# Kernel tuning notes

Hardware: AMD Instinct MI355X
Metric: run time of the kernel (lower is better)

The kernel has to match this reference:

```python
import jax, jax.numpy as jnp
import numpy as np

B, H, W, DIM = 1, 256, 256, 192
HEADS = 6
K, DIL = 7, 2            # NAttention kernel / dilation
WS, DF = 8, 2            # stripe window size, anchor down factor
AWS = WS // DF           # anchor window size (4)
N1, N2 = WS * WS, AWS * AWS
L = H * W
CPB_HID = 512


def _nbr(size, k, d):
    # 1D neighborhood-attention neighbor indices with dilation (edge-clamped)
    i = np.arange(size); g = i % d; p = i // d
    gsize = size // d  # d divides size
    start = np.clip(p - k // 2, 0, gsize - k)
    nbr_p = start[:, None] + np.arange(k)[None, :]
    nbr = g[:, None] + d * nbr_p                    # absolute key index
    rb = nbr_p - p[:, None] + (k - 1)               # rpb index in [0, 2k-2]
    return nbr.astype(np.int32), rb.astype(np.int32)

NBR_H, RB_H = _nbr(H, K, DIL)
NBR_W, RB_W = _nbr(W, K, DIL)


def _na_attention(q, k, v, rpb):
    # q,k,v: (B, heads, H, W, hd); rpb: (heads, 2K-1, 2K-1)
    bias = rpb[:, RB_H, :]                          # (heads,H,K,2K-1)
    bias = jnp.take(bias, RB_W, axis=3)             # (heads,H,K,W,K)
    bias = jnp.transpose(bias, (0, 1, 3, 2, 4))     # (heads,H,W,K,K)
    logits = []
    for ki in range(K):
        kh = jnp.take(k, NBR_H[:, ki], axis=2)
        for kj in range(K):
            khw = jnp.take(kh, NBR_W[:, kj], axis=3)
            logits.append(jnp.einsum('bnhwc,bnhwc->bnhw', q, khw))
    a = jnp.stack(logits, axis=-1).reshape(*q.shape[:4], K, K) + bias[None]
    a = jax.nn.softmax(a.reshape(*q.shape[:4], K * K), axis=-1).reshape(*q.shape[:4], K, K)
    out = jnp.zeros_like(q)
    for ki in range(K):
        vh = jnp.take(v, NBR_H[:, ki], axis=2)
        for kj in range(K):
            vhw = jnp.take(vh, NBR_W[:, kj], axis=3)
            out = out + a[..., ki, kj, None] * vhw
    return out

na_attention = jax.checkpoint(_na_attention)


def window_partition(x, ws):
    b, h, w, c = x.shape
    x = x.reshape(b, h // ws, ws, w // ws, ws, c)
    return jnp.transpose(x, (0, 1, 3, 2, 4, 5)).reshape(-1, ws * ws, c)


def window_reverse(x, ws, h, w):
    c = x.shape[-1]
    b = x.shape[0] // ((h // ws) * (w // ws))
    x = x.reshape(b, h // ws, w // ws, ws, ws, c)
    return jnp.transpose(x, (0, 1, 3, 2, 4, 5)).reshape(b, h, w, c)


def _l2n(x):
    n = jnp.linalg.norm(x, axis=-1, keepdims=True)
    return x / jnp.maximum(n, 1e-12)


def _affine(attn, table, index, ls, w1, b1, w2):
    # attn: (Bw, heads, Na, Nb)
    attn = attn * jnp.exp(jnp.minimum(ls, float(np.log(100.0))))[None]
    bt = jax.nn.relu(table.reshape(-1, 2) @ w1 + b1) @ w2           # (T, heads)
    bias = bt[index.reshape(-1)].reshape(index.shape[0], index.shape[1], HEADS)
    bias = 16.0 * jax.nn.sigmoid(jnp.transpose(bias, (2, 0, 1)))    # (heads,Na,Nb)
    return attn + bias[None]


def _cos_attn(q, k, v, table, index, ls, w1, b1, w2):
    attn = jnp.einsum('bhnc,bhmc->bhnm', _l2n(q), _l2n(k))
    attn = jax.nn.softmax(_affine(attn, table, index, ls, w1, b1, w2), axis=-1)
    return attn @ v


def _forward(x, h_size, w_size, table, index_a2w, index_w2a, qkv_w, qkv_b,
             anchor_dw_w, anchor_dw_b, anchor_pw_w, anchor_pw_b,
             na_qkv_w, na_qkv_b, na_after_w, na_after_b, na_rpb,
             ls1, cpb1_w1, cpb1_b1, cpb1_w2, ls2, cpb2_w1, cpb2_b1, cpb2_w2,
             proj_w, proj_b):
    Bx, Lx, C = x.shape
    Hs, Ws_ = int(h_size), int(w_size)
    qkv = x @ qkv_w + qkv_b                     # (B,L,3C)
    half = C * 3 // 2
    qkv_window, qkv_stripe = qkv[..., :half], qkv[..., half:]
    # anchor projection: depthwise conv (k=DF+1, stride=DF) + pointwise
    xi = x.reshape(Bx, Hs, Ws_, C)
    a = jax.lax.conv_general_dilated(
        xi, anchor_dw_w, (DF, DF), ((1, 1), (1, 1)),
        dimension_numbers=('NHWC', 'HWIO', 'NHWC'), feature_group_count=C) + anchor_dw_b
    a = a @ anchor_pw_w + anchor_pw_b           # (B, H/DF, W/DF, C//2)
    # ---- neighborhood attention branch ----
    hd = C // HEADS
    xw = qkv_window.reshape(Bx, Hs, Ws_, half)
    q2 = (xw @ na_qkv_w + na_qkv_b).reshape(Bx, Hs, Ws_, 3, HEADS, hd)
    q2 = jnp.transpose(q2, (3, 0, 4, 1, 2, 5))  # (3,B,heads,H,W,hd)
    qn, kn, vn = q2[0] * hd ** -0.5, q2[1], q2[2]
    xna = na_attention(qn, kn, vn, na_rpb)
    xna = jnp.transpose(xna, (0, 2, 3, 1, 4)).reshape(Bx, Hs, Ws_, C)
    xna = (xna @ na_after_w + na_after_b).reshape(Bx, Lx, C // 2)
    # ---- anchor stripe attention branch ----
    qs = window_partition(qkv_stripe.reshape(Bx, Hs, Ws_, half), WS)  # (Bw,N1,1.5C)
    an = window_partition(a, AWS)                                     # (Bw,N2,C//2)
    Bw = qs.shape[0]
    hs = C // 2 // HEADS
    q3 = jnp.transpose(qs.reshape(Bw, N1, 3, HEADS, hs), (2, 0, 3, 1, 4))
    q_s, k_s, v_s = q3[0], q3[1], q3[2]
    an = jnp.transpose(an.reshape(Bw, N2, HEADS, hs), (0, 2, 1, 3))
    x1 = _cos_attn(an, k_s, v_s, table, index_a2w, ls1, cpb1_w1, cpb1_b1, cpb1_w2)
    x2 = _cos_attn(q_s, an, x1, table, index_w2a, ls2, cpb2_w1, cpb2_b1, cpb2_w2)
    x2 = jnp.transpose(x2, (0, 2, 1, 3)).reshape(Bw, N1, C // 2)
    xs = window_reverse(x2, WS, Hs, Ws_).reshape(Bx, Lx, C // 2)
    return jnp.concatenate([xna, xs], axis=-1) @ proj_w + proj_b


def setup_inputs() -> dict:
    key = jax.random.key(0)
    ks = jax.random.split(key, 16)
    f = lambda i, shp, s=0.02: jax.random.normal(ks[i], shp, dtype=jnp.float32) * s
    x = jax.random.normal(ks[0], (B, L, DIM), dtype=jnp.float32)
    # swin-v2 style normalized log-spaced relative coords table
    rc = np.arange(-(WS - 1), WS, dtype=np.float32) / (WS - 1)
    t = np.stack(np.meshgrid(rc, rc, indexing='ij'), axis=-1)[None]
    table = jnp.asarray(np.sign(t) * np.log2(1 + np.abs(t) * 8) / 3.0, dtype=jnp.float32)
    wc = np.arange(WS); ac = np.arange(AWS) * DF
    cw = np.stack(np.meshgrid(wc, wc, indexing='ij'), -1).reshape(-1, 2)
    ca = np.stack(np.meshgrid(ac, ac, indexing='ij'), -1).reshape(-1, 2)
    def _idx(c1, c2):
        d = c1[:, None, :] - c2[None, :, :]
        return jnp.asarray((d[..., 0] + WS - 1) * (2 * WS - 1) + (d[..., 1] + WS - 1), dtype=jnp.int32)
    return {
        'x': x, 'h_size': H, 'w_size': W, 'table': table,
        'index_a2w': _idx(ca, cw), 'index_w2a': _idx(cw, ca),
        'qkv_w': f(1, (DIM, 3 * DIM)), 'qkv_b': jnp.zeros((3 * DIM,), jnp.float32),
        'anchor_dw_w': f(2, (DF + 1, DF + 1, 1, DIM), 0.1),
        'anchor_dw_b': jnp.zeros((DIM,), jnp.float32),
        'anchor_pw_w': f(3, (DIM, DIM // 2)), 'anchor_pw_b': jnp.zeros((DIM // 2,), jnp.float32),
        'na_qkv_w': f(4, (3 * DIM // 2, 3 * DIM)), 'na_qkv_b': jnp.zeros((3 * DIM,), jnp.float32),
        'na_after_w': f(5, (DIM, DIM // 2)), 'na_after_b': jnp.zeros((DIM // 2,), jnp.float32),
        'na_rpb': f(6, (HEADS, 2 * K - 1, 2 * K - 1)),
        'ls1': jnp.log(10.0) * jnp.ones((HEADS, 1, 1), jnp.float32),
        'cpb1_w1': f(7, (2, CPB_HID), 0.1), 'cpb1_b1': jnp.zeros((CPB_HID,), jnp.float32),
        'cpb1_w2': f(8, (CPB_HID, HEADS), 0.1),
        'ls2': jnp.log(10.0) * jnp.ones((HEADS, 1, 1), jnp.float32),
        'cpb2_w1': f(9, (2, CPB_HID), 0.1), 'cpb2_b1': jnp.zeros((CPB_HID,), jnp.float32),
        'cpb2_w2': f(10, (CPB_HID, HEADS), 0.1),
        'proj_w': f(11, (DIM, DIM)), 'proj_b': jnp.zeros((DIM,), jnp.float32),
    }


def reference(x, h_size, w_size, table, index_a2w, index_w2a, qkv_w, qkv_b,
              anchor_dw_w, anchor_dw_b, anchor_pw_w, anchor_pw_b,
              na_qkv_w, na_qkv_b, na_after_w, na_after_b, na_rpb,
              ls1, cpb1_w1, cpb1_b1, cpb1_w2, ls2, cpb2_w1, cpb2_b1, cpb2_w2,
              proj_w, proj_b):
    return _forward(x, h_size, w_size, table, index_a2w, index_w2a, qkv_w, qkv_b,
                    anchor_dw_w, anchor_dw_b, anchor_pw_w, anchor_pw_b,
                    na_qkv_w, na_qkv_b, na_after_w, na_after_b, na_rpb,
                    ls1, cpb1_w1, cpb1_b1, cpb1_w2, ls2, cpb2_w1, cpb2_b1, cpb2_w2,
                    proj_w, proj_b)
```

## Files before the change

kernel.cpp:

```cpp
#include <hip/hip_runtime.h>
#include <math.h>


typedef unsigned short bf16_t;
typedef __attribute__((ext_vector_type(8))) short short8;
typedef __attribute__((ext_vector_type(4))) float f32x4;

__device__ inline float bf2f(bf16_t v) { return __uint_as_float((unsigned)v << 16); }
__device__ inline bf16_t f2bf(float f) {
    unsigned u = __float_as_uint(f);
    unsigned r = (u + 0x7fffu + ((u >> 16) & 1u)) >> 16;
    return (bf16_t)r;
}
__device__ inline float cvt(float v) { return v; }
__device__ inline float cvt(bf16_t v) { return bf2f(v); }
__device__ inline void sto(float* p, float v) { *p = v; }
__device__ inline void sto(bf16_t* p, float v) { *p = f2bf(v); }

__device__ inline void ld_bf8(const bf16_t* p, float* d) {
    uint4 r = *(const uint4*)p;
    d[0] = __uint_as_float(r.x << 16); d[1] = __uint_as_float(r.x & 0xffff0000u);
    d[2] = __uint_as_float(r.y << 16); d[3] = __uint_as_float(r.y & 0xffff0000u);
    d[4] = __uint_as_float(r.z << 16); d[5] = __uint_as_float(r.z & 0xffff0000u);
    d[6] = __uint_as_float(r.w << 16); d[7] = __uint_as_float(r.w & 0xffff0000u);
}
__device__ inline unsigned pk2(float a, float b) {
    return (unsigned)f2bf(a) | ((unsigned)f2bf(b) << 16);
}

template <int KD, int NA, typename TO>
__global__ __launch_bounds__(256) void mfma_gemm_k(
    const bf16_t* __restrict__ A, const bf16_t* __restrict__ Bt,
    const float* __restrict__ bias, TO* __restrict__ C,
    int lda, int ldb, int ldc)
{
    const int t = threadIdx.x;
    const int lane = t & 63, wave = t >> 6;
    const int wr = wave >> 1, wc = wave & 1;
    const int m0 = blockIdx.y * 128 + wr * 64;
    const int n0 = blockIdx.x * 96 + wc * 48;
    const int lm = lane & 15;
    const int q  = lane >> 4;

    f32x4 acc[4][3] = {};
    const bf16_t* ap = A + (size_t)(m0 + lm) * lda + q * 8;
    const bf16_t* bp = Bt + (size_t)(n0 + lm) * ldb + q * 8;

#pragma unroll
    for (int k0 = 0; k0 < KD; k0 += 32) {
        short8 af[4], bf[3];
#pragma unroll
        for (int mi = 0; mi < 4; mi++)
            af[mi] = *(const short8*)(ap + (size_t)(mi * 16) * lda + k0);
#pragma unroll
        for (int ni = 0; ni < 3; ni++)
            bf[ni] = *(const short8*)(bp + (size_t)(ni * 16) * ldb + k0);
#pragma unroll
        for (int mi = 0; mi < 4; mi++)
#pragma unroll
            for (int ni = 0; ni < 3; ni++)
                acc[mi][ni] = __builtin_amdgcn_mfma_f32_16x16x32_bf16(
                    af[mi], bf[ni], acc[mi][ni], 0, 0, 0);
    }

#pragma unroll
    for (int mi = 0; mi < 4; mi++) {
#pragma unroll
        for (int ni = 0; ni < 3; ni++) {
            int col = n0 + ni * 16 + lm;
            float bv = bias[col];
            if (NA) {
                int which = col / 192;
                int hh = (col % 192) / 32;
                int d  = col % 32;
#pragma unroll
                for (int r = 0; r < 4; r++) {
                    int row = m0 + mi * 16 + q * 4 + r;
                    int ii = row >> 8, jj = row & 255;
                    int par = ((ii & 1) << 1) | (jj & 1);
                    int pixin = (ii >> 1) * 128 + (jj >> 1);
                    size_t addr;
                    if (which == 2)
                        addr = (((size_t)(12 + hh) * 4 + par) << 19)
                             + ((size_t)d << 14) + pixin;
                    else
                        addr = ((size_t)which * 6 + hh) * 2097152 + d
                             + ((size_t)(par * 16384 + pixin) << 5);
                    sto(&C[addr], acc[mi][ni][r] + bv);
                }
            } else {
#pragma unroll
                for (int r = 0; r < 4; r++) {
                    int row = m0 + mi * 16 + q * 4 + r;
                    sto(&C[(size_t)row * ldc + col], acc[mi][ni][r] + bv);
                }
            }
        }
    }
}

__global__ __launch_bounds__(256) void cvt_bf16_k(
    const float* __restrict__ src, bf16_t* __restrict__ dst, int n8)
{
    int tid = blockIdx.x * 256 + threadIdx.x;
    if (tid >= n8) return;
    float4 a = ((const float4*)src)[tid * 2];
    float4 b = ((const float4*)src)[tid * 2 + 1];
    uint4 o;
    o.x = pk2(a.x, a.y); o.y = pk2(a.z, a.w);
    o.z = pk2(b.x, b.y); o.w = pk2(b.z, b.w);
    ((uint4*)dst)[tid] = o;
}

__global__ __launch_bounds__(256) void tcvt_k(
    const float* __restrict__ W, bf16_t* __restrict__ Wt,
    int Kd, int N, int ld, int coloff)
{
    int tid = blockIdx.x * 256 + threadIdx.x;
    if (tid >= Kd * N) return;
    int k = tid % Kd, n = tid / Kd;
    Wt[tid] = f2bf(W[(size_t)k * ld + coloff + n]);
}

__global__ __launch_bounds__(256) void tpose_qkvw_k(
    const float* __restrict__ W, float* __restrict__ WT)
{
    int tid = blockIdx.x * 256 + threadIdx.x;
    if (tid >= 288 * 192) return;
    int k = tid % 192, j = tid / 192;
    WT[tid] = W[(size_t)k * 576 + j];
}

__global__ __launch_bounds__(256) void fold_wna_t_k(
    const float* __restrict__ qkv_wT, const float* __restrict__ na_qkv_w,
    bf16_t* __restrict__ Wna_t)
{
    int tid = blockIdx.x * 256 + threadIdx.x;
    if (tid >= 576 * 192) return;
    int k = tid % 192, n = tid / 192;
    float acc = 0.f;
    for (int j = 0; j < 288; j++)
        acc += qkv_wT[j * 192 + k] * na_qkv_w[j * 576 + n];
    Wna_t[tid] = f2bf(acc);
}

__global__ __launch_bounds__(256) void fold_bna_k(
    const float* __restrict__ qkv_b, const float* __restrict__ na_qkv_w,
    const float* __restrict__ na_qkv_b, float* __restrict__ bna)
{
    int j = blockIdx.x * 256 + threadIdx.x;
    if (j >= 576) return;
    float acc = na_qkv_b[j];
    for (int k = 0; k < 288; k++)
        acc += qkv_b[k] * na_qkv_w[k * 576 + j];
    bna[j] = acc;
}

__global__ __launch_bounds__(256) void cpb_k(
    const float* __restrict__ table, const float* __restrict__ w1,
    const float* __restrict__ b1, const float* __restrict__ w2,
    float* __restrict__ bt)
{
    int tid = blockIdx.x * 256 + threadIdx.x;
    if (tid >= 225 * 6) return;
    int h = tid % 6, t = tid / 6;
    float t0 = table[t * 2], t1 = table[t * 2 + 1];
    float acc = 0.f;
    for (int m = 0; m < 512; m++) {
        float hv = t0 * w1[m] + t1 * w1[512 + m] + b1[m];
        hv = fmaxf(hv, 0.f);
        acc += hv * w2[m * 6 + h];
    }
    bt[tid] = acc;
}

__global__ __launch_bounds__(256) void sigb_k(
    const float* __restrict__ bt, const int* __restrict__ idx,
    float* __restrict__ bp)
{
    int tid = blockIdx.x * 256 + threadIdx.x;
    if (tid >= 6144) return;
    int h = tid >> 10, p = tid & 1023;
    bp[tid] = 16.0f / (1.0f + __expf(-bt[idx[p] * 6 + h]));
}

__global__ __launch_bounds__(256) void sigb1T_k(
    const float* __restrict__ bt, const int* __restrict__ idx,
    float* __restrict__ bp)
{
    int tid = blockIdx.x * 256 + threadIdx.x;
    if (tid >= 6144) return;
    int h = tid >> 10, p = tid & 1023;
    int m = p >> 4, n2 = p & 15;
    bp[tid] = 16.0f / (1.0f + __expf(-bt[idx[n2 * 64 + m] * 6 + h]));
}

#define BM 64
#define BN 64
#define BKK 16
template <typename TA, typename TO>
__global__ __launch_bounds__(256) void gemm_k(
    const TA* __restrict__ A, const float* __restrict__ B,
    const float* __restrict__ bias, TO* __restrict__ C,
    int M, int N, int Kd, int lda, int ldb, int ldc)
{
    __shared__ float As[BKK][BM + 1];
    __shared__ float Bs[BKK][BN + 1];
    const int t  = threadIdx.x;
    const int tx = t & 15, ty = t >> 4;
    const int m0 = blockIdx.y * BM, n0 = blockIdx.x * BN;
    float acc[4][4] = {};

    for (int k0 = 0; k0 < Kd; k0 += BKK) {
#pragma unroll
        for (int i = 0; i < 4; i++) {
            int m = (t >> 4) + i * 16;
            int k = t & 15;
            int gm = m0 + m, gk = k0 + k;
            As[k][m] = (gm < M && gk < Kd) ? cvt(A[(size_t)gm * lda + gk]) : 0.f;
        }
#pragma unroll
        for (int i = 0; i < 4; i++) {
            int k = (t >> 6) + i * 4;
            int n = t & 63;
            int gk = k0 + k, gn = n0 + n;
            Bs[k][n] = (gk < Kd && gn < N) ? B[(size_t)gk * ldb + gn] : 0.f;
        }
        __syncthreads();
#pragma unroll
        for (int k = 0; k < BKK; k++) {
            float a[4], b[4];
#pragma unroll
            for (int i = 0; i < 4; i++) a[i] = As[k][ty * 4 + i];
#pragma unroll
            for (int j = 0; j < 4; j++) b[j] = Bs[k][tx * 4 + j];
#pragma unroll
            for (int i = 0; i < 4; i++)
#pragma unroll
                for (int j = 0; j < 4; j++) acc[i][j] += a[i] * b[j];
        }
        __syncthreads();
    }
#pragma unroll
    for (int i = 0; i < 4; i++) {
        int gm = m0 + ty * 4 + i;
        if (gm >= M) continue;
#pragma unroll
        for (int j = 0; j < 4; j++) {
            int gn = n0 + tx * 4 + j;
            if (gn >= N) continue;
            sto(&C[(size_t)gm * ldc + gn], acc[i][j] + bias[gn]);
        }
    }
}

__global__ __launch_bounds__(256) void dwconv_k(
    const float* __restrict__ x, const float* __restrict__ w,
    const float* __restrict__ b, float* __restrict__ adw)
{
    int tid = blockIdx.x * 256 + threadIdx.x;
    if (tid >= 16384 * 48) return;
    int c4 = tid % 48;
    int p = tid / 48;
    int ow = p & 127, oh = p >> 7;
    int c = c4 * 4;
    float4 s = *(const float4*)(b + c);
#pragma unroll
    for (int kh = 0; kh < 3; kh++) {
        int ih = oh * 2 - 1 + kh;
        if (ih < 0 || ih >= 256) continue;
#pragma unroll
        for (int kw = 0; kw < 3; kw++) {
            int iw = ow * 2 - 1 + kw;
            if (iw < 0 || iw >= 256) continue;
            float4 xv = *(const float4*)(x + (size_t)(ih * 256 + iw) * 192 + c);
            float4 wv = *(const float4*)(w + (kh * 3 + kw) * 192 + c);
            s.x += xv.x * wv.x; s.y += xv.y * wv.y;
            s.z += xv.z * wv.z; s.w += xv.w * wv.w;
        }
    }
    *(float4*)(adw + (size_t)p * 192 + c) = s;
}

__global__ __launch_bounds__(256) void na_attn_k(
    const bf16_t* __restrict__ nap, const float* __restrict__ rpb,
    bf16_t* __restrict__ outp)
{
    __shared__ float rpb_s[176];
    __shared__ __align__(16) unsigned P_s[4][16][20];

    const int bid  = blockIdx.x;
    const int work = (bid & 7) * 768 + (bid >> 3);
    const int z    = work >> 8;
    const int rem  = work & 255;
    const int pi   = rem >> 1;
    const int xh   = rem & 1;

    const int t = threadIdx.x;
    const int wv = t >> 6, lane = t & 63;
    const int lm = lane & 15, lq = lane >> 4;
    const int h = z >> 2, par = z & 3;

    if (t < 169) rpb_s[t] = rpb[h * 169 + t];
    __syncthreads();

    const int pj0 = xh * 64 + wv * 16;
    const int si  = min(max(pi - 3, 0), 121);
    const int rbh0 = si - pi + 6;
    const int c0  = min(max(pj0 - 3, 0), 121) & ~7;

    const size_t plane = (size_t)65536 * 32;
    const size_t poff  = (size_t)(par * 16384) * 32;
    const bf16_t* qpl = nap + (size_t)h * plane + poff;
    const bf16_t* kpl = nap + (size_t)(6 + h) * plane + poff;
    const bf16_t* vtpl = nap + (((size_t)(12 + h) * 4 + par) << 19);

    const short8 qf = *(const short8*)(qpl + ((size_t)(pi * 128 + pj0 + lm)) * 32 + lq * 8);

    int offc[4][2]; bool vm[4][2];
#pragma unroll
    for (int r = 0; r < 4; r++) {
        int q = lq * 4 + r, pj = pj0 + q;
        int sj = min(max(pj - 3, 0), 121);
#pragma unroll
        for (int t2 = 0; t2 < 2; t2++) {
            int c = c0 + 2 * lm + t2;
            vm[r][t2] = (c >= sj) && (c <= sj + 6);
            offc[r][t2] = min(max(c - pj + 6, 0), 12);
        }
    }
    const int kc0 = min(c0 + 2 * lm,     127) * 64;
    const int kc1 = min(c0 + 2 * lm + 1, 127) * 64;
    const int vcol = c0 + (lq << 3);
    const size_t vb0 = (size_t)lm * 16384;
    const size_t vb1 = (size_t)(lm + 16) * 16384;

    const float scale = 0.17677669529663687f;
    f32x4 o0 = {}, o1 = {};
    float sums[4] = {0.f, 0.f, 0.f, 0.f};
    const f32x4 zz = {};

#pragma unroll 2
    for (int rr = 0; rr < 7; rr++) {
        const char* krow = (const char*)kpl + (size_t)((si + rr) * 128) * 64;

        short8 kf0 = *(const short8*)(krow + kc0 + lq * 16);
        short8 kf1 = *(const short8*)(krow + kc1 + lq * 16);
        f32x4 s0 = __builtin_amdgcn_mfma_f32_16x16x32_bf16(qf, kf0, zz, 0, 0, 0);
        f32x4 s1 = __builtin_amdgcn_mfma_f32_16x16x32_bf16(qf, kf1, zz, 0, 0, 0);

        const float* br = rpb_s + (rbh0 + rr) * 13;
        float e0[4], e1[4];
#pragma unroll
        for (int r = 0; r < 4; r++) {
            float a0 = __expf(fmaf(s0[r], scale, br[offc[r][0]]));
            float a1 = __expf(fmaf(s1[r], scale, br[offc[r][1]]));
            a0 = vm[r][0] ? a0 : 0.f;
            a1 = vm[r][1] ? a1 : 0.f;
            e0[r] = a0; e1[r] = a1;
            sums[r] += a0 + a1;
        }
#pragma unroll
        for (int r = 0; r < 4; r++) {
            unsigned pr;
            asm("v_cvt_pk_bf16_f32 %0, %1, %2" : "=v"(pr) : "v"(e0[r]), "v"(e1[r]));
            P_s[wv][lq * 4 + r][lm] = pr;
        }
        const short8 pf = *(const short8*)((const bf16_t*)P_s[wv][lm] + lq * 8);

        int rowo = min((si + rr) * 128 + vcol, 16376);
        short8 vf0 = *(const short8*)(vtpl + vb0 + rowo);
        short8 vf1 = *(const short8*)(vtpl + vb1 + rowo);

        o0 = __builtin_amdgcn_mfma_f32_16x16x32_bf16(pf, vf0, o0, 0, 0, 0);
        o1 = __builtin_amdgcn_mfma_f32_16x16x32_bf16(pf, vf1, o1, 0, 0, 0);
    }

#pragma unroll
    for (int r = 0; r < 4; r++) {
        float s = sums[r];
        s += __shfl_xor(s, 1, 64);
        s += __shfl_xor(s, 2, 64);
        s += __shfl_xor(s, 4, 64);
        s += __shfl_xor(s, 8, 64);
        sums[r] = 1.0f / s;
    }

    const int gi = par >> 1, gj = par & 1;
    const int i0 = pi * 2 + gi;
    bf16_t* ob = outp + ((size_t)i0 * 256 + gj) * 192 + h * 32 + lm;
#pragma unroll
    for (int r = 0; r < 4; r++) {
        int q = lq * 4 + r;
        size_t px = (size_t)(pj0 + q) * 2 * 192;
        ob[px]      = f2bf(o0[r] * sums[r]);
        ob[px + 16] = f2bf(o1[r] * sums[r]);
    }
}

__global__ __launch_bounds__(256) void attn1_k(
    const float* __restrict__ apw,
    const bf16_t* __restrict__ qkvs,
    const float* __restrict__ b1pT,
    const float* __restrict__ ls1,
    float* __restrict__ x1)
{
    __shared__ float bT_s[1024];
    __shared__ __align__(16) unsigned P_s[4][16][36];

    const int t = threadIdx.x;
    const int wv = t >> 6, lane = t & 63;
    const int lm = lane & 15, lq = lane >> 4;
    const int h = blockIdx.y;
    const int w = blockIdx.x * 4 + wv;
    const int wi = w >> 5, wj = w & 31;

#pragma unroll
    for (int i = 0; i < 4; i++) bT_s[i * 256 + t] = b1pT[h * 1024 + i * 256 + t];
    __syncthreads();

    const float scale = __expf(fminf(ls1[h], 4.605170185988091f));

    short8 af = {};
    float an2 = 0.f;
    {
        int ay = wi * 4 + (lm >> 2), ax = wj * 4 + (lm & 3);
        const float* ap = apw + (size_t)(ay * 128 + ax) * 96 + h * 16;
        if (lq < 2) {
            float4 v0 = *(const float4*)(ap + lq * 8);
            float4 v1 = *(const float4*)(ap + lq * 8 + 4);
            float vs[8] = {v0.x, v0.y, v0.z, v0.w, v1.x, v1.y, v1.z, v1.w};
            unsigned* au = (unsigned*)&af;
#pragma unroll
            for (int j2 = 0; j2 < 4; j2++) {
                unsigned u = pk2(vs[2 * j2], vs[2 * j2 + 1]);
                au[j2] = u;
                float lo = __uint_as_float(u << 16);
                float hi = __uint_as_float(u & 0xffff0000u);
                an2 += lo * lo + hi * hi;
            }
        }
    }
    an2 += __shfl_xor(an2, 16, 64);
    an2 += __shfl_xor(an2, 32, 64);
    const float sa = scale / fmaxf(sqrtf(an2), 1e-12f);

    const f32x4 zz = {};
    f32x4 o = {};
    float sum = 0.f;

#pragma unroll
    for (int g = 0; g < 2; g++) {
#pragma unroll
        for (int tt = 0; tt < 2; tt++) {
            const int tile = g * 2 + tt;
            int py = wi * 8 + tile * 2 + (lm >> 3);
            int px = wj * 8 + (lm & 7);
            const bf16_t* kp = qkvs + (size_t)(py * 256 + px) * 288 + 96 + h * 16;
            short8 kf = {};
            float kn2 = 0.f;
            float klo[4], khi[4];
            if (lq < 2) {
                uint4 kr = *(const uint4*)(kp + lq * 8);
                unsigned ku[4] = {kr.x, kr.y, kr.z, kr.w};
#pragma unroll
                for (int j2 = 0; j2 < 4; j2++) {
                    klo[j2] = __uint_as_float(ku[j2] << 16);
                    khi[j2] = __uint_as_float(ku[j2] & 0xffff0000u);
                    kn2 += klo[j2] * klo[j2] + khi[j2] * khi[j2];
                }
            }
            kn2 += __shfl_xor(kn2, 16, 64);
            kn2 += __shfl_xor(kn2, 32, 64);
            float rk = 1.0f / fmaxf(sqrtf(kn2), 1e-12f);
            if (lq < 2) {
                unsigned* kuo = (unsigned*)&kf;
#pragma unroll
                for (int j2 = 0; j2 < 4; j2++)
                    kuo[j2] = pk2(klo[j2] * rk, khi[j2] * rk);
            }
            f32x4 s = __builtin_amdgcn_mfma_f32_16x16x32_bf16(kf, af, zz, 0, 0, 0);
            float e[4];
#pragma unroll
            for (int r = 0; r < 4; r++) {
                e[r] = __expf(fmaf(s[r], sa,
                              bT_s[((tile * 16 + lq * 4 + r) << 4) + lm]));
                sum += e[r];
            }
            P_s[wv][lm][tile * 8 + lq * 2]     = pk2(e[0], e[1]);
            P_s[wv][lm][tile * 8 + lq * 2 + 1] = pk2(e[2], e[3]);
        }
        const short8 pf = *(const short8*)&P_s[wv][lm][g * 16 + lq * 4];
        short8 vf;
        int pyv = wi * 8 + g * 4 + lq;
        const bf16_t* vrow = qkvs + (size_t)(pyv * 256 + wj * 8) * 288 + 192 + h * 16 + lm;
#pragma unroll
        for (int i = 0; i < 8; i++)
            ((bf16_t*)&vf)[i] = vrow[(size_t)i * 288];
        o = __builtin_amdgcn_mfma_f32_16x16x32_bf16(pf, vf, o, 0, 0, 0);
    }

    sum += __shfl_xor(sum, 16, 64);
    sum += __shfl_xor(sum, 32, 64);
    const float inv = 1.0f / sum;
    float* xp = x1 + ((size_t)w * 6 + h) * 256;
#pragma unroll
    for (int r = 0; r < 4; r++) {
        float iv = __shfl(inv, lq * 4 + r, 64);
        xp[(lq * 4 + r) * 16 + lm] = o[r] * iv;
    }
}

__global__ __launch_bounds__(256) void attn2_k(
    const float* __restrict__ apw,
    const bf16_t* __restrict__ qkvs,
    const float* __restrict__ b2p,
    const float* __restrict__ ls2,
    const float* __restrict__ x1,
    bf16_t* __restrict__ cat)
{
    int tid = blockIdx.x * 256 + threadIdx.x;
    if (tid >= 1024 * 6 * 64) return;
    int n1 = tid & 63;
    int h = (tid >> 6) % 6;
    int w = tid / 384;
    int wi = w >> 5, wj = w & 31;
    float scale = __expf(fminf(ls2[h], 4.605170185988091f));

    int qy = wi * 8 + (n1 >> 3), qx = wj * 8 + (n1 & 7);
    const bf16_t* qp = qkvs + (size_t)(qy * 256 + qx) * 288 + h * 16;
    float qv[16];
    ld_bf8(qp, qv); ld_bf8(qp + 8, qv + 8);
    float nrm = 0.f;
#pragma unroll
    for (int d = 0; d < 16; d++) nrm += qv[d] * qv[d];
    float innorm = 1.0f / fmaxf(sqrtf(nrm), 1e-12f);
#pragma unroll
    for (int d = 0; d < 16; d++) qv[d] *= innorm;

    const float* bp = b2p + h * 1024 + n1 * 16;
    float sum = 0.f;
    float acc[16] = {};
#pragma unroll
    for (int m = 0; m < 16; m++) {
        int ay = wi * 4 + (m >> 2), ax = wj * 4 + (m & 3);
        const float* ap = apw + (size_t)(ay * 128 + ax) * 96 + h * 16;
        float dot = 0.f, kn = 0.f;
#pragma unroll
        for (int d = 0; d < 16; d += 4) {
            float4 v = *(const float4*)(ap + d);
            dot += qv[d] * v.x + qv[d + 1] * v.y + qv[d + 2] * v.z + qv[d + 3] * v.w;
            kn += v.x * v.x + v.y * v.y + v.z * v.z + v.w * v.w;
        }
        dot *= 1.0f / fmaxf(sqrtf(kn), 1e-12f);
        float e = __expf(fmaf(dot, scale, bp[m]));
        sum += e;
        const float* vp = x1 + ((size_t)w * 6 + h) * 256 + m * 16;
#pragma unroll
        for (int d = 0; d < 16; d += 4) {
            float4 v = *(const float4*)(vp + d);
            acc[d] += e * v.x; acc[d + 1] += e * v.y;
            acc[d + 2] += e * v.z; acc[d + 3] += e * v.w;
        }
    }
    float inv = 1.0f / sum;
#pragma unroll
    for (int d = 0; d < 16; d++) acc[d] *= inv;
    bf16_t* op = cat + (size_t)(qy * 256 + qx) * 192 + 96 + h * 16;
    uint4 o0, o1;
    o0.x = pk2(acc[0], acc[1]);   o0.y = pk2(acc[2], acc[3]);
    o0.z = pk2(acc[4], acc[5]);   o0.w = pk2(acc[6], acc[7]);
    o1.x = pk2(acc[8], acc[9]);   o1.y = pk2(acc[10], acc[11]);
    o1.z = pk2(acc[12], acc[13]); o1.w = pk2(acc[14], acc[15]);
    *(uint4*)(op) = o0;
    *(uint4*)(op + 8) = o1;
}

extern "C" void kernel_launch(void* const* d_in, const int* in_sizes, int n_in,
                              void* d_out, int out_size, void* d_ws, size_t ws_size,
                              hipStream_t stream) {
    const float* x          = (const float*)d_in[0];
    const float* table      = (const float*)d_in[3];
    const int*   idx_a2w    = (const int*)d_in[4];
    const int*   idx_w2a    = (const int*)d_in[5];
    const float* qkv_w      = (const float*)d_in[6];
    const float* qkv_b      = (const float*)d_in[7];
    const float* adw_w      = (const float*)d_in[8];
    const float* adw_b      = (const float*)d_in[9];
    const float* apw_w      = (const float*)d_in[10];
    const float* apw_b      = (const float*)d_in[11];
    const float* na_qkv_w   = (const float*)d_in[12];
    const float* na_qkv_b   = (const float*)d_in[13];
    const float* na_after_w = (const float*)d_in[14];
    const float* na_after_b = (const float*)d_in[15];
    const float* na_rpb     = (const float*)d_in[16];
    const float* ls1        = (const float*)d_in[17];
    const float* cpb1_w1    = (const float*)d_in[18];
    const float* cpb1_b1    = (const float*)d_in[19];
    const float* cpb1_w2    = (const float*)d_in[20];
    const float* ls2        = (const float*)d_in[21];
    const float* cpb2_w1    = (const float*)d_in[22];
    const float* cpb2_b1    = (const float*)d_in[23];
    const float* cpb2_w2    = (const float*)d_in[24];
    const float* proj_w     = (const float*)d_in[25];
    const float* proj_b     = (const float*)d_in[26];
    float* out = (float*)d_out;
    (void)in_sizes; (void)n_in; (void)out_size; (void)ws_size;

    char* base = (char*)d_ws;
    size_t off = 0;
    auto alloc = [&](size_t bytes) {
        off = (off + 255) & ~(size_t)255;
        void* p = base + off; off += bytes; return p;
    };
    float*  bna    = (float*)alloc(576 * 4);
    float*  bt1    = (float*)alloc(225 * 6 * 4);
    float*  bt2    = (float*)alloc(225 * 6 * 4);
    float*  b1pT   = (float*)alloc(6144 * 4);
    float*  b2p    = (float*)alloc(6144 * 4);
    float*  qkv_wT = (float*)alloc(288 * 192 * 4);
    bf16_t* Wna_t  = (bf16_t*)alloc(576 * 192 * 2);
    bf16_t* Ws_t   = (bf16_t*)alloc(288 * 192 * 2);
    bf16_t* Waft_t = (bf16_t*)alloc(96 * 192 * 2);
    bf16_t* Wproj_t= (bf16_t*)alloc(192 * 192 * 2);
    bf16_t* qkvs   = (bf16_t*)alloc((size_t)65536 * 288 * 2);
    char*   naR    = (char*)alloc((size_t)65536 * 576 * 2);
    char*   R      = (char*)alloc((size_t)65536 * 192 * 2);
    float*  apw    = (float*)alloc((size_t)16384 * 96 * 4);
    bf16_t* naqkv   = (bf16_t*)naR;
    float*  x1      = (float*)naR;
    bf16_t* cat     = (bf16_t*)(naR + (8 << 20));
    bf16_t* xb      = (bf16_t*)R;
    float*  adw     = (float*)R;
    bf16_t* xna_pre = (bf16_t*)R;

    tpose_qkvw_k<<<216, 256, 0, stream>>>(qkv_w, qkv_wT);
    fold_wna_t_k<<<432, 256, 0, stream>>>(qkv_wT, na_qkv_w, Wna_t);
    fold_bna_k<<<3, 256, 0, stream>>>(qkv_b, na_qkv_w, na_qkv_b, bna);
    cpb_k<<<6, 256, 0, stream>>>(table, cpb1_w1, cpb1_b1, cpb1_w2, bt1);
    cpb_k<<<6, 256, 0, stream>>>(table, cpb2_w1, cpb2_b1, cpb2_w2, bt2);
    sigb1T_k<<<24, 256, 0, stream>>>(bt1, idx_a2w, b1pT);
    sigb_k<<<24, 256, 0, stream>>>(bt2, idx_w2a, b2p);
    tcvt_k<<<216, 256, 0, stream>>>(qkv_w, Ws_t, 192, 288, 576, 288);
    tcvt_k<<<72, 256, 0, stream>>>(na_after_w, Waft_t, 192, 96, 96, 0);
    tcvt_k<<<144, 256, 0, stream>>>(proj_w, Wproj_t, 192, 192, 192, 0);
    cvt_bf16_k<<<6144, 256, 0, stream>>>(x, xb, 65536 * 192 / 8);

    mfma_gemm_k<192, 0, bf16_t><<<dim3(3, 512), 256, 0, stream>>>(
        xb, Ws_t, qkv_b + 288, qkvs, 192, 192, 288);

    mfma_gemm_k<192, 1, bf16_t><<<dim3(6, 512), 256, 0, stream>>>(
        xb, Wna_t, bna, naqkv, 192, 192, 576);

    dwconv_k<<<3072, 256, 0, stream>>>(x, adw_w, adw_b, adw);
    gemm_k<float, float><<<dim3(2, 256), 256, 0, stream>>>(
        adw, apw_w, apw_b, apw, 16384, 96, 192, 192, 96, 96);

    na_attn_k<<<6144, 256, 0, stream>>>(naqkv, na_rpb, xna_pre);

    mfma_gemm_k<192, 0, bf16_t><<<dim3(1, 512), 256, 0, stream>>>(
        xna_pre, Waft_t, na_after_b, cat, 192, 192, 192);

    attn1_k<<<dim3(256, 6), 256, 0, stream>>>(apw, qkvs, b1pT, ls1, x1);
    attn2_k<<<1536, 256, 0, stream>>>(apw, qkvs, b2p, ls2, x1, cat);

    mfma_gemm_k<192, 0, float><<<dim3(2, 512), 256, 0, stream>>>(
        cat, Wproj_t, proj_b, out, 192, 192, 192);
}
```

Baseline: 638.8 us.

## Write V in pixel-major layout and transpose via separate LDS kernel; swizzle GEMM blocks

The NA qkv GEMM epilogue no longer scatters V directly into a d-major transposed layout with 2-byte strided stores. It writes V like Q/K, and a new shared-memory transpose kernel produces the transposed V into the output buffer, which is used as scratch. All MFMA GEMMs also switch to a 1D grid remapped so that consecutive blocks spread across XCDs. This trades an extra read and write pass over V for coalesced stores in the GEMM epilogue.

```diff
diff --git a/kernel.cpp b/kernel.cpp
--- a/kernel.cpp
+++ b/kernel.cpp
@@ -28,17 +28,22 @@
     return (unsigned)f2bf(a) | ((unsigned)f2bf(b) << 16);
 }
 
-template <int KD, int NA, typename TO>
+template <int KD, int NA, int NCOL, typename TO>
 __global__ __launch_bounds__(256) void mfma_gemm_k(
     const bf16_t* __restrict__ A, const bf16_t* __restrict__ Bt,
     const float* __restrict__ bias, TO* __restrict__ C,
     int lda, int ldb, int ldc)
 {
+    const int bid  = blockIdx.x;
+    const int work = (bid & 7) * (gridDim.x >> 3) + (bid >> 3);
+    const int brow = work / NCOL;
+    const int bcol = work - brow * NCOL;
+
     const int t = threadIdx.x;
     const int lane = t & 63, wave = t >> 6;
     const int wr = wave >> 1, wc = wave & 1;
-    const int m0 = blockIdx.y * 128 + wr * 64;
-    const int n0 = blockIdx.x * 96 + wc * 48;
+    const int m0 = brow * 128 + wr * 64;
+    const int n0 = bcol * 96 + wc * 48;
     const int lm = lane & 15;
     const int q  = lane >> 4;
 
@@ -73,20 +78,15 @@
                 int which = col / 192;
                 int hh = (col % 192) / 32;
                 int d  = col % 32;
+                size_t pbase = ((size_t)which * 6 + hh) * 2097152 + d;
 #pragma unroll
                 for (int r = 0; r < 4; r++) {
                     int row = m0 + mi * 16 + q * 4 + r;
                     int ii = row >> 8, jj = row & 255;
                     int par = ((ii & 1) << 1) | (jj & 1);
                     int pixin = (ii >> 1) * 128 + (jj >> 1);
-                    size_t addr;
-                    if (which == 2)
-                        addr = (((size_t)(12 + hh) * 4 + par) << 19)
-                             + ((size_t)d << 14) + pixin;
-                    else
-                        addr = ((size_t)which * 6 + hh) * 2097152 + d
-                             + ((size_t)(par * 16384 + pixin) << 5);
-                    sto(&C[addr], acc[mi][ni][r] + bv);
+                    sto(&C[pbase + ((size_t)(par * 16384 + pixin) << 5)],
+                        acc[mi][ni][r] + bv);
                 }
             } else {
 #pragma unroll
@@ -96,6 +96,42 @@
                 }
             }
         }
+    }
+}
+
+__global__ __launch_bounds__(256) void vtpose_k(
+    const bf16_t* __restrict__ nap, bf16_t* __restrict__ vt)
+{
+    __shared__ unsigned short tl[32][144];
+    const int b = blockIdx.x;
+    const int z = b >> 7;
+    const int tile = b & 127;
+    const int h = z >> 2, par = z & 3;
+    const int pix0 = tile << 7;
+
+    const bf16_t* sp = nap + (size_t)(12 + h) * 2097152
+                     + ((size_t)(par * 16384 + pix0) << 5);
+    const int t = threadIdx.x;
+    {
+        const int px = t & 127, half = t >> 7;
+        uint4 r0 = *(const uint4*)(sp + px * 32 + half * 16);
+        uint4 r1 = *(const uint4*)(sp + px * 32 + half * 16 + 8);
+        const unsigned short* u0 = (const unsigned short*)&r0;
+        const unsigned short* u1 = (const unsigned short*)&r1;
+#pragma unroll
+        for (int i = 0; i < 8; i++) tl[half * 16 + i][px] = u0[i];
+#pragma unroll
+        for (int i = 0; i < 8; i++) tl[half * 16 + 8 + i][px] = u1[i];
+    }
+    __syncthreads();
+    {
+        const int d = t >> 3, g = t & 7;
+        unsigned short buf[16];
+#pragma unroll
+        for (int i = 0; i < 16; i++) buf[i] = tl[d][g * 16 + i];
+        bf16_t* dp = vt + ((size_t)z << 19) + ((size_t)d << 14) + pix0 + g * 16;
+        *(uint4*)dp = *(uint4*)buf;
+        *(uint4*)(dp + 8) = *(uint4*)(buf + 8);
     }
 }
 
@@ -283,8 +319,8 @@
 }
 
 __global__ __launch_bounds__(256) void na_attn_k(
-    const bf16_t* __restrict__ nap, const float* __restrict__ rpb,
-    bf16_t* __restrict__ outp)
+    const bf16_t* __restrict__ nap, const bf16_t* __restrict__ vt,
+    const float* __restrict__ rpb, bf16_t* __restrict__ outp)
 {
     __shared__ float rpb_s[176];
     __shared__ __align__(16) unsigned P_s[4][16][20];
@@ -313,7 +349,7 @@
     const size_t poff  = (size_t)(par * 16384) * 32;
     const bf16_t* qpl = nap + (size_t)h * plane + poff;
     const bf16_t* kpl = nap + (size_t)(6 + h) * plane + poff;
-    const bf16_t* vtpl = nap + (((size_t)(12 + h) * 4 + par) << 19);
+    const bf16_t* vtpl = vt + ((size_t)z << 19);
 
     const short8 qf = *(const short8*)(qpl + ((size_t)(pi * 128 + pj0 + lm)) * 32 + lq * 8);
 
@@ -633,6 +669,7 @@
     bf16_t* xb      = (bf16_t*)R;
     float*  adw     = (float*)R;
     bf16_t* xna_pre = (bf16_t*)R;
+    bf16_t* vt      = (bf16_t*)out;
 
     tpose_qkvw_k<<<216, 256, 0, stream>>>(qkv_w, qkv_wT);
     fold_wna_t_k<<<432, 256, 0, stream>>>(qkv_wT, na_qkv_w, Wna_t);
@@ -646,24 +683,26 @@
     tcvt_k<<<144, 256, 0, stream>>>(proj_w, Wproj_t, 192, 192, 192, 0);
     cvt_bf16_k<<<6144, 256, 0, stream>>>(x, xb, 65536 * 192 / 8);
 
-    mfma_gemm_k<192, 0, bf16_t><<<dim3(3, 512), 256, 0, stream>>>(
+    mfma_gemm_k<192, 0, 3, bf16_t><<<1536, 256, 0, stream>>>(
         xb, Ws_t, qkv_b + 288, qkvs, 192, 192, 288);
 
-    mfma_gemm_k<192, 1, bf16_t><<<dim3(6, 512), 256, 0, stream>>>(
+    mfma_gemm_k<192, 1, 6, bf16_t><<<3072, 256, 0, stream>>>(
         xb, Wna_t, bna, naqkv, 192, 192, 576);
+
+    vtpose_k<<<3072, 256, 0, stream>>>(naqkv, vt);
 
     dwconv_k<<<3072, 256, 0, stream>>>(x, adw_w, adw_b, adw);
     gemm_k<float, float><<<dim3(2, 256), 256, 0, stream>>>(
         adw, apw_w, apw_b, apw, 16384, 96, 192, 192, 96, 96);
 
-    na_attn_k<<<6144, 256, 0, stream>>>(naqkv, na_rpb, xna_pre);
-
-    mfma_gemm_k<192, 0, bf16_t><<<dim3(1, 512), 256, 0, stream>>>(
+    na_attn_k<<<6144, 256, 0, stream>>>(naqkv, vt, na_rpb, xna_pre);
+
+    mfma_gemm_k<192, 0, 1, bf16_t><<<512, 256, 0, stream>>>(
         xna_pre, Waft_t, na_after_b, cat, 192, 192, 192);
 
     attn1_k<<<dim3(256, 6), 256, 0, stream>>>(apw, qkvs, b1pT, ls1, x1);
     attn2_k<<<1536, 256, 0, stream>>>(apw, qkvs, b2p, ls2, x1, cat);
 
-    mfma_gemm_k<192, 0, float><<<dim3(2, 512), 256, 0, stream>>>(
+    mfma_gemm_k<192, 0, 2, float><<<1024, 256, 0, stream>>>(
         cat, Wproj_t, proj_b, out, 192, 192, 192);
 }
```

Result: faster. 613.8 us (-3.9%).
